# Kernel optimization log

Hardware: AMD Instinct MI355X
Metric: run time of the kernel (lower is better)

Reference implementation:

```python
import jax, jax.numpy as jnp
import numpy as np

WINDOW = 4
EPS = 1e-5


def setup_inputs() -> dict:
    key = jax.random.key(0)
    ks = jax.random.split(key, 12)
    B, T, D = 2, 4096, 1024
    H = D // 2
    s = 0.02
    return {
        "x": jax.random.normal(ks[0], (B, T, D), dtype=jnp.float32),
        # tension_net: Linear(2D -> D/2), SiLU, Linear(D/2 -> 1). Weights stored [in, out].
        "w1": jax.random.normal(ks[1], (2 * D, H), dtype=jnp.float32) * s,
        "b1": jnp.zeros((H,), dtype=jnp.float32),
        "w2": jax.random.normal(ks[2], (H, 1), dtype=jnp.float32) * s,
        "b2": jnp.zeros((1,), dtype=jnp.float32),
        # wv: Linear(D -> D)
        "wv_w": jax.random.normal(ks[3], (D, D), dtype=jnp.float32) * s,
        "wv_b": jnp.zeros((D,), dtype=jnp.float32),
        # merge: Linear(2D -> D)
        "merge_w": jax.random.normal(ks[4], (2 * D, D), dtype=jnp.float32) * s,
        "merge_b": jnp.zeros((D,), dtype=jnp.float32),
        # LayerNorm(D)
        "gamma": jnp.ones((D,), dtype=jnp.float32),
        "beta": jnp.zeros((D,), dtype=jnp.float32),
    }


def reference(x, w1, b1, w2, b2, wv_w, wv_b, merge_w, merge_b, gamma, beta):
    B, T, D = x.shape
    W = WINDOW
    # Causal sliding-window neighbor gather: nb[:, t, w] = x[:, t-w-1] if t-w-1 >= 0 else 0.
    idx = jnp.arange(T)[:, None] - jnp.arange(W)[None, :] - 1          # [T, W]
    valid = (idx >= 0)                                                  # [T, W]
    nb = jnp.take(x, jnp.clip(idx, 0, None), axis=1)                   # [B, T, W, D]
    nb = jnp.where(valid[None, :, :, None], nb, jnp.zeros((), x.dtype))
    # Pairwise tension gate: tiny MLP on [h_t, nb].
    h_t = jnp.broadcast_to(x[:, :, None, :], (B, T, W, D))
    pair = jnp.concatenate([h_t, nb], axis=-1)                          # [B, T, W, 2D]
    hid = jax.nn.silu(jnp.einsum('btwe,eh->btwh', pair, w1) + b1)       # [B, T, W, D/2]
    tau = jax.nn.sigmoid((jnp.einsum('btwh,ho->btwo', hid, w2) + b2)[..., 0])  # [B, T, W]
    # Value projection of neighbors (note: zero-padded neighbors still get wv bias, matching torch).
    v = jnp.einsum('btwd,de->btwe', nb, wv_w) + wv_b                    # [B, T, W, D]
    msg = jnp.einsum('btw,btwd->btd', tau, v)                           # [B, T, D]
    # Merge + LayerNorm.
    y = jnp.einsum('bte,ed->btd', jnp.concatenate([x, msg], axis=-1), merge_w) + merge_b
    mu = jnp.mean(y, axis=-1, keepdims=True)
    var = jnp.mean(jnp.square(y - mu), axis=-1, keepdims=True)
    y = (y - mu) * jax.lax.rsqrt(var + EPS) * gamma + beta
    return y
```

## Files before the change

kernel.cpp:

```cpp
#include <hip/hip_runtime.h>
#include <hip/hip_bf16.h>

#define TT 4096
#define TD 1024
#define TM 8192
#define CN 3072
#define EPS 1e-5f

typedef __bf16 bf16;
typedef __bf16 bf16x4 __attribute__((ext_vector_type(4)));
typedef __bf16 bf16x8 __attribute__((ext_vector_type(8)));
typedef float  f32x4  __attribute__((ext_vector_type(4)));

#define GLOBAL_AS __attribute__((address_space(1)))
#define LDS_AS    __attribute__((address_space(3)))

__global__ __launch_bounds__(256) void prep_kernel(const float* __restrict__ x,
                                                   const float* __restrict__ w1,
                                                   const float* __restrict__ wv_w,
                                                   const float* __restrict__ wv_b,
                                                   const float* __restrict__ merge_w,
                                                   bf16* __restrict__ Xbf,
                                                   bf16* __restrict__ BigBT,
                                                   bf16* __restrict__ Amb,
                                                   bf16* __restrict__ WvBf,
                                                   float* __restrict__ cvecP) {
    __shared__ float tile[32][33];
    int b = blockIdx.x;
    const int tid = threadIdx.x;

    if (b < 16) {
        const int j = (b & 3) * 256 + tid;
        const int e0 = (b >> 2) * 256;
        const float* col = merge_w + (size_t)(1024 + e0) * 1024 + j;
        float acc = 0.f;
#pragma unroll 32
        for (int e = 0; e < 256; ++e) acc += wv_b[e0 + e] * col[(size_t)e * 1024];
        cvecP[(b >> 2) * 1024 + j] = acc;
        return;
    }
    b -= 16;
    if (b < 8192) {
        int i = b * 256 + tid;
        float4 v = ((const float4*)x)[i];
        bf16x4 o; o[0] = (bf16)v.x; o[1] = (bf16)v.y; o[2] = (bf16)v.z; o[3] = (bf16)v.w;
        *(bf16x4*)(Xbf + (size_t)i * 4) = o;
        return;
    }
    b -= 8192;

    const float* src; bf16* dst; int srcN, tilesX, dstOff;
    if (b < 512)       {            src = w1;                        srcN = 512;  tilesX = 16; dst = BigBT; dstOff = 0;    }
    else if (b < 1024) { b -= 512;  src = w1 + (size_t)1024 * 512;   srcN = 512;  tilesX = 16; dst = BigBT; dstOff = 512;  }
    else if (b < 2048) { b -= 1024; src = merge_w;                   srcN = 1024; tilesX = 32; dst = BigBT; dstOff = 2048; }
    else if (b < 3072) { b -= 2048; src = merge_w + (size_t)1024 * 1024; srcN = 1024; tilesX = 32; dst = Amb; dstOff = 0; }
    else {
        b -= 3072;
        int i = b * 256 + tid;
        float4 v = ((const float4*)wv_w)[i];
        bf16x4 o; o[0] = (bf16)v.x; o[1] = (bf16)v.y; o[2] = (bf16)v.z; o[3] = (bf16)v.w;
        *(bf16x4*)(WvBf + (size_t)i * 4) = o;
        return;
    }
    int n0 = (b % tilesX) * 32, k0 = (b / tilesX) * 32;
    int tx = tid & 31, ty = tid >> 5;
#pragma unroll
    for (int r = 0; r < 32; r += 8)
        tile[ty + r][tx] = src[(size_t)(k0 + ty + r) * srcN + n0 + tx];
    __syncthreads();
#pragma unroll
    for (int r = 0; r < 32; r += 8)
        dst[(size_t)(dstOff + n0 + ty + r) * 1024 + k0 + tx] = (bf16)tile[tx][ty + r];
}

__global__ __launch_bounds__(256) void wprime_kernel(const bf16* __restrict__ Amb,
                                                     const bf16* __restrict__ WvBf,
                                                     bf16* __restrict__ Wout,
                                                     const float* __restrict__ cvecP,
                                                     float* __restrict__ cvec) {
    int b = blockIdx.x;
    if (b == 256) {
        int j = threadIdx.x * 4;
        float4 s0 = *(const float4*)(cvecP + j);
        float4 s1 = *(const float4*)(cvecP + 1024 + j);
        float4 s2 = *(const float4*)(cvecP + 2048 + j);
        float4 s3 = *(const float4*)(cvecP + 3072 + j);
        float4 o = {s0.x + s1.x + s2.x + s3.x, s0.y + s1.y + s2.y + s3.y,
                    s0.z + s1.z + s2.z + s3.z, s0.w + s1.w + s2.w + s3.w};
        *(float4*)(cvec + j) = o;
        return;
    }
    __shared__ bf16 As[64 * 64];
    __shared__ bf16 Bs[64 * 64];
    const int m0 = (b >> 4) * 64;
    const int n0 = (b & 15) * 64;
    const int tid = threadIdx.x;
    const int wave = tid >> 6, lane = tid & 63;
    const int wr = (wave >> 1) * 32, wc = (wave & 1) * 32;
    const int lrow = lane & 15, cbase = lane >> 4;
    const int sw = lrow & 7;

    f32x4 acc[2][2] = {};

    for (int k0 = 0; k0 < 1024; k0 += 64) {
        __syncthreads();
#pragma unroll
        for (int c = 0; c < 2; ++c) {
            int e = (c * 256 + tid) * 8;
            int row = e >> 6;
            int q = (e >> 3) & 7;
            int gcol = ((q ^ (row & 7)) << 3);
            const bf16* ga = Amb  + (size_t)(m0 + row) * 1024 + k0 + gcol;
            const bf16* gb = WvBf + (size_t)(n0 + row) * 1024 + k0 + gcol;
            __builtin_amdgcn_global_load_lds((const GLOBAL_AS void*)ga,
                                             (LDS_AS void*)(As + e), 16, 0, 0);
            __builtin_amdgcn_global_load_lds((const GLOBAL_AS void*)gb,
                                             (LDS_AS void*)(Bs + e), 16, 0, 0);
        }
        __syncthreads();

#pragma unroll
        for (int kk = 0; kk < 2; ++kk) {
            const int qo = ((cbase + kk * 4) ^ sw) << 3;
            bf16x8 af[2], bfr[2];
#pragma unroll
            for (int i = 0; i < 2; ++i) {
                af[i]  = *(const bf16x8*)(As + (wr + i * 16 + lrow) * 64 + qo);
                bfr[i] = *(const bf16x8*)(Bs + (wc + i * 16 + lrow) * 64 + qo);
            }
#pragma unroll
            for (int i = 0; i < 2; ++i)
#pragma unroll
                for (int j = 0; j < 2; ++j)
                    acc[i][j] = __builtin_amdgcn_mfma_f32_16x16x32_bf16(af[i], bfr[j], acc[i][j], 0, 0, 0);
        }
    }

    const int lr = (lane >> 4) * 4, lc = lane & 15;
#pragma unroll
    for (int i = 0; i < 2; ++i)
#pragma unroll
        for (int j = 0; j < 2; ++j)
#pragma unroll
            for (int r = 0; r < 4; ++r)
                Wout[(size_t)(m0 + wr + i * 16 + lr + r) * 1024 + (n0 + wc + j * 16 + lc)]
                    = (bf16)acc[i][j][r];
}

#define STAGE_A(T, kh) do {                                                       \
    bf16* base_ = SMEM + ((T) & 1) * 16384 + (kh) * 8192;                         \
    _Pragma("unroll")                                                             \
    for (int ld = 0; ld < 2; ++ld) {                                              \
        int e_ = (ld * 512 + tid) * 8;                                            \
        int row_ = e_ >> 5;                                                       \
        int q2_ = (e_ >> 3) & 3;                                                  \
        int gcol_ = ((q2_ ^ (row_ & 3)) << 3);                                    \
        const bf16* ga_ = A + (size_t)(m0 + row_) * K + (T) * 64 + (kh) * 32 + gcol_; \
        __builtin_amdgcn_global_load_lds((const GLOBAL_AS void*)ga_,              \
                                         (LDS_AS void*)(base_ + e_), 16, 0, 0);   \
    } } while (0)

#define STAGE_B(T) do {                                                           \
    bf16* base_ = SMEM + 32768 + ((T) & 1) * 12288;                               \
    _Pragma("unroll")                                                             \
    for (int ld = 0; ld < 3; ++ld) {                                              \
        int e_ = (ld * 512 + tid) * 8;                                            \
        int row_ = e_ >> 6;                                                       \
        int q_ = (e_ >> 3) & 7;                                                   \
        int gcol_ = ((q_ ^ (row_ & 7)) << 3);                                     \
        const bf16* gb_ = BT + (size_t)(n0 + row_) * K + (T) * 64 + gcol_;        \
        __builtin_amdgcn_global_load_lds((const GLOBAL_AS void*)gb_,              \
                                         (LDS_AS void*)(base_ + e_), 16, 0, 0);   \
    } } while (0)

#define NOSTAGE do {} while (0)
#define NOGATE  do {} while (0)
#define GATE2 do { asm volatile("s_waitcnt vmcnt(2)" ::: "memory");               \
                   __builtin_amdgcn_sched_barrier(0); } while (0)
#define GATE0 do { asm volatile("s_waitcnt vmcnt(0)" ::: "memory");               \
                   __builtin_amdgcn_sched_barrier(0); } while (0)

#define PHASE(tt, kk, ih, STAGE, GATE) do {                                       \
    bf16x8 af0 = *(const bf16x8*)(SMEM + (tt) * 16384 + (kk) * 8192 +             \
                                  (wm * 64 + (ih) * 32 + lrow) * 32 + aqo);       \
    bf16x8 af1 = *(const bf16x8*)(SMEM + (tt) * 16384 + (kk) * 8192 +             \
                                  (wm * 64 + (ih) * 32 + 16 + lrow) * 32 + aqo);  \
    if ((ih) == 0) {                                                              \
        _Pragma("unroll")                                                         \
        for (int j = 0; j < 6; ++j)                                               \
            bfr[j] = *(const bf16x8*)(SMEM + 32768 + (tt) * 12288 +               \
                                      (wn * 96 + j * 16 + lrow) * 64 +            \
                                      (((cbase + (kk) * 4) ^ sw) << 3));          \
    }                                                                             \
    STAGE;                                                                        \
    __builtin_amdgcn_s_barrier();                                                 \
    __builtin_amdgcn_sched_barrier(0);                                            \
    __builtin_amdgcn_s_setprio(1);                                                \
    _Pragma("unroll")                                                             \
    for (int j = 0; j < 6; ++j) {                                                 \
        acc[(ih) * 2][j]     = __builtin_amdgcn_mfma_f32_16x16x32_bf16(           \
                                   af0, bfr[j], acc[(ih) * 2][j], 0, 0, 0);       \
        acc[(ih) * 2 + 1][j] = __builtin_amdgcn_mfma_f32_16x16x32_bf16(           \
                                   af1, bfr[j], acc[(ih) * 2 + 1][j], 0, 0, 0);   \
    }                                                                             \
    __builtin_amdgcn_s_setprio(0);                                                \
    GATE;                                                                         \
    __builtin_amdgcn_s_barrier();                                                 \
    __builtin_amdgcn_sched_barrier(0);                                            \
} while (0)

__global__ __launch_bounds__(512, 2) void gemm_big(const bf16* __restrict__ A,
                                                   const bf16* __restrict__ BT,
                                                   bf16* __restrict__ C) {
    __shared__ __align__(16) bf16 SMEM[57344];
    const int NB = 3072, K = 1024;

    int L = blockIdx.y * 16 + blockIdx.x;
    int tile = (L & 7) * 64 + (L >> 3);
    const int m0 = (tile >> 4) * 256;
    const int n0 = (tile & 15) * 192;
    const int tid = threadIdx.x;
    const int wave = tid >> 6, lane = tid & 63;
    const int wm = wave >> 1;
    const int wn = wave & 1;
    const int lrow = lane & 15, cbase = lane >> 4;
    const int sw = lrow & 7;
    const int aqo = ((cbase ^ (lrow & 3)) << 3);

    f32x4 acc[4][6] = {};
    bf16x8 bfr[6];

    STAGE_A(0, 0);
    STAGE_A(0, 1);
    STAGE_B(0);
    STAGE_A(1, 0);
    asm volatile("s_waitcnt vmcnt(2)" ::: "memory");
    __builtin_amdgcn_sched_barrier(0);
    __builtin_amdgcn_s_barrier();
    __builtin_amdgcn_sched_barrier(0);

    for (int i = 0; i < 7; ++i) {
        const int t1 = 2 * i + 1, t2 = 2 * i + 2, t3 = 2 * i + 3;
        PHASE(0, 0, 0, STAGE_A(t1, 1), NOGATE);
        PHASE(0, 0, 1, STAGE_B(t1),    NOGATE);
        PHASE(0, 1, 0, STAGE_A(t2, 0), NOGATE);
        PHASE(0, 1, 1, NOSTAGE,        GATE2);
        PHASE(1, 0, 0, STAGE_A(t2, 1), NOGATE);
        PHASE(1, 0, 1, STAGE_B(t2),    NOGATE);
        PHASE(1, 1, 0, STAGE_A(t3, 0), NOGATE);
        PHASE(1, 1, 1, NOSTAGE,        GATE2);
    }
    PHASE(0, 0, 0, STAGE_A(15, 1), NOGATE);
    PHASE(0, 0, 1, STAGE_B(15),    NOGATE);
    PHASE(0, 1, 0, NOSTAGE,        NOGATE);
    PHASE(0, 1, 1, NOSTAGE,        GATE0);
    PHASE(1, 0, 0, NOSTAGE,        NOGATE);
    PHASE(1, 0, 1, NOSTAGE,        NOGATE);
    PHASE(1, 1, 0, NOSTAGE,        NOGATE);
    PHASE(1, 1, 1, NOSTAGE,        NOGATE);

    __syncthreads();
    bf16* ep = SMEM + wave * 6656;
    const int lr = (lane >> 4) * 4, lc = lane & 15;
#pragma unroll
    for (int i = 0; i < 4; ++i)
#pragma unroll
        for (int j = 0; j < 6; ++j)
#pragma unroll
            for (int r = 0; r < 4; ++r)
                ep[(i * 16 + lr + r) * 104 + (j * 16 + lc)] = (bf16)acc[i][j][r];
    __syncthreads();

    bf16* Cw = C + (size_t)(m0 + wm * 64) * NB + n0 + wn * 96;
#pragma unroll
    for (int p = 0; p < 8; ++p) {
        int R = p * 8 + (lane >> 3);
        int Ccol = (lane & 7) * 8;
        bf16x8 v = *(const bf16x8*)(ep + R * 104 + Ccol);
        *(bf16x8*)(Cw + (size_t)R * NB + Ccol) = v;
    }
#pragma unroll
    for (int p = 0; p < 4; ++p) {
        int R = p * 16 + (lane >> 2);
        int Ccol = 64 + (lane & 3) * 8;
        bf16x8 v = *(const bf16x8*)(ep + R * 104 + Ccol);
        *(bf16x8*)(Cw + (size_t)R * NB + Ccol) = v;
    }
}

__global__ __launch_bounds__(256) void final_kernel(const bf16* __restrict__ C,
                                                    const float* __restrict__ b1,
                                                    const float* __restrict__ b2,
                                                    const float* __restrict__ w2,
                                                    const float* __restrict__ cvec,
                                                    const float* __restrict__ merge_b,
                                                    const float* __restrict__ gamma,
                                                    const float* __restrict__ beta,
                                                    float* __restrict__ out) {
    const int wave = threadIdx.x >> 6, lane = threadIdx.x & 63;
    const int row = blockIdx.x * 4 + wave;
    const int t = row & (TT - 1);
    const bf16* Crow = C + (size_t)row * CN;

    const int h0 = lane * 8;
    bf16x8 u8 = *(const bf16x8*)(Crow + h0);
    float4 b1a = *(const float4*)(b1 + h0), b1b = *(const float4*)(b1 + h0 + 4);
    float4 w2a = *(const float4*)(w2 + h0), w2b = *(const float4*)(w2 + h0 + 4);
    float u[8] = {(float)u8[0] + b1a.x, (float)u8[1] + b1a.y,
                  (float)u8[2] + b1a.z, (float)u8[3] + b1a.w,
                  (float)u8[4] + b1b.x, (float)u8[5] + b1b.y,
                  (float)u8[6] + b1b.z, (float)u8[7] + b1b.w};
    const float w2v[8] = {w2a.x, w2a.y, w2a.z, w2a.w, w2b.x, w2b.y, w2b.z, w2b.w};

    float partial[4];
#pragma unroll
    for (int w = 0; w < 4; ++w) {
        float p = 0.f;
        if (t >= w + 1) {
            bf16x8 v8 = *(const bf16x8*)(C + (size_t)(row - w - 1) * CN + 512 + h0);
#pragma unroll
            for (int k = 0; k < 8; ++k) {
                float z = u[k] + (float)v8[k];
                p += (z / (1.f + __expf(-z))) * w2v[k];
            }
        } else {
#pragma unroll
            for (int k = 0; k < 8; ++k) {
                float z = u[k];
                p += (z / (1.f + __expf(-z))) * w2v[k];
            }
        }
        partial[w] = p;
    }
#pragma unroll
    for (int w = 0; w < 4; ++w)
#pragma unroll
        for (int off = 1; off < 64; off <<= 1)
            partial[w] += __shfl_xor(partial[w], off, 64);

    const float bias2 = b2[0];
    float taus[4];
#pragma unroll
    for (int w = 0; w < 4; ++w)
        taus[w] = 1.f / (1.f + __expf(-(partial[w] + bias2)));
    const float tsum = taus[0] + taus[1] + taus[2] + taus[3];

    const int d0 = lane * 16;
    bf16x8 y1a = *(const bf16x8*)(Crow + 2048 + d0);
    bf16x8 y1b = *(const bf16x8*)(Crow + 2048 + d0 + 8);
    float v[16];
#pragma unroll
    for (int k = 0; k < 8; ++k) { v[k] = (float)y1a[k]; v[8 + k] = (float)y1b[k]; }
#pragma unroll
    for (int q = 0; q < 4; ++q) {
        float4 cv = *(const float4*)(cvec + d0 + q * 4);
        float4 mb = *(const float4*)(merge_b + d0 + q * 4);
        v[q*4+0] += tsum * cv.x + mb.x; v[q*4+1] += tsum * cv.y + mb.y;
        v[q*4+2] += tsum * cv.z + mb.z; v[q*4+3] += tsum * cv.w + mb.w;
    }
#pragma unroll
    for (int w = 0; w < 4; ++w) {
        if (t >= w + 1) {
            const bf16* Pn = C + (size_t)(row - w - 1) * CN + 1024 + d0;
            bf16x8 pa = *(const bf16x8*)Pn;
            bf16x8 pb = *(const bf16x8*)(Pn + 8);
#pragma unroll
            for (int k = 0; k < 8; ++k) {
                v[k] += taus[w] * (float)pa[k];
                v[8 + k] += taus[w] * (float)pb[k];
            }
        }
    }

    float s = 0.f, ss = 0.f;
#pragma unroll
    for (int k = 0; k < 16; ++k) { s += v[k]; ss += v[k] * v[k]; }
#pragma unroll
    for (int off = 1; off < 64; off <<= 1) {
        s  += __shfl_xor(s, off, 64);
        ss += __shfl_xor(ss, off, 64);
    }
    const float mu = s * (1.f / TD);
    const float var = ss * (1.f / TD) - mu * mu;
    const float r = rsqrtf(var + EPS);

#pragma unroll
    for (int q = 0; q < 4; ++q) {
        float4 g  = *(const float4*)(gamma + d0 + q * 4);
        float4 bt = *(const float4*)(beta + d0 + q * 4);
        float4 o;
        o.x = (v[q*4+0] - mu) * r * g.x + bt.x;
        o.y = (v[q*4+1] - mu) * r * g.y + bt.y;
        o.z = (v[q*4+2] - mu) * r * g.z + bt.z;
        o.w = (v[q*4+3] - mu) * r * g.w + bt.w;
        *(float4*)(out + (size_t)row * TD + d0 + q * 4) = o;
    }
}

extern "C" void kernel_launch(void* const* d_in, const int* in_sizes, int n_in,
                              void* d_out, int out_size, void* d_ws, size_t ws_size,
                              hipStream_t stream) {
    const float* x       = (const float*)d_in[0];
    const float* w1      = (const float*)d_in[1];
    const float* b1      = (const float*)d_in[2];
    const float* w2      = (const float*)d_in[3];
    const float* b2      = (const float*)d_in[4];
    const float* wv_w    = (const float*)d_in[5];
    const float* wv_b    = (const float*)d_in[6];
    const float* merge_w = (const float*)d_in[7];
    const float* merge_b = (const float*)d_in[8];
    const float* gamma   = (const float*)d_in[9];
    const float* beta    = (const float*)d_in[10];
    float* out = (float*)d_out;

    char* ws = (char*)d_ws;
    bf16*  Xbf   = (bf16*)ws;  ws += (size_t)TM * 1024 * 2;
    bf16*  BigBT = (bf16*)ws;  ws += (size_t)CN * 1024 * 2;
    bf16*  Amb   = (bf16*)ws;  ws += (size_t)1024 * 1024 * 2;
    bf16*  WvBf  = (bf16*)ws;  ws += (size_t)1024 * 1024 * 2;
    float* cvecP = (float*)ws; ws += (size_t)4 * 1024 * 4;
    float* cvec  = (float*)ws; ws += (size_t)1024 * 4;
    bf16*  Cbuf  = (bf16*)ws;

    prep_kernel<<<12304, 256, 0, stream>>>(x, w1, wv_w, wv_b, merge_w,
                                           Xbf, BigBT, Amb, WvBf, cvecP);

    wprime_kernel<<<257, 256, 0, stream>>>(Amb, WvBf, BigBT + (size_t)1024 * 1024,
                                           cvecP, cvec);

    gemm_big<<<dim3(16, 32), 512, 0, stream>>>(Xbf, BigBT, Cbuf);

    final_kernel<<<TM / 4, 256, 0, stream>>>(Cbuf, b1, b2, w2, cvec, merge_b,
                                             gamma, beta, out);
}
```

Baseline: 202.7 us.

## Enlarge big GEMM tile to 256x384 with full-K-tile double buffering

```diff
diff --git a/kernel.cpp b/kernel.cpp
--- a/kernel.cpp
+++ b/kernel.cpp
@@ -147,61 +147,53 @@
                     = (bf16)acc[i][j][r];
 }
 
-#define STAGE_A(T, kh) do {                                                       \
-    bf16* base_ = SMEM + ((T) & 1) * 16384 + (kh) * 8192;                         \
+#define MFMA16(a, b, c) __builtin_amdgcn_mfma_f32_16x16x32_bf16((a), (b), (c), 0, 0, 0)
+
+#define STAGE_A(BUF, T) do {                                                      \
     _Pragma("unroll")                                                             \
-    for (int ld = 0; ld < 2; ++ld) {                                              \
-        int e_ = (ld * 512 + tid) * 8;                                            \
-        int row_ = e_ >> 5;                                                       \
-        int q2_ = (e_ >> 3) & 3;                                                  \
-        int gcol_ = ((q2_ ^ (row_ & 3)) << 3);                                    \
-        const bf16* ga_ = A + (size_t)(m0 + row_) * K + (T) * 64 + (kh) * 32 + gcol_; \
+    for (int ld_ = 0; ld_ < 4; ++ld_) {                                           \
+        const bf16* ga_ = aBase + (size_t)(ld_ * 64) * 1024 + (T) * 64;           \
         __builtin_amdgcn_global_load_lds((const GLOBAL_AS void*)ga_,              \
-                                         (LDS_AS void*)(base_ + e_), 16, 0, 0);   \
+            (LDS_AS void*)(SMEM + (BUF) * 40960 + ld_ * 4096 + tid * 8), 16, 0, 0); \
     } } while (0)
 
-#define STAGE_B(T) do {                                                           \
-    bf16* base_ = SMEM + 32768 + ((T) & 1) * 12288;                               \
+#define STAGE_B(BUF, T, L0, L1) do {                                              \
     _Pragma("unroll")                                                             \
-    for (int ld = 0; ld < 3; ++ld) {                                              \
-        int e_ = (ld * 512 + tid) * 8;                                            \
-        int row_ = e_ >> 6;                                                       \
-        int q_ = (e_ >> 3) & 7;                                                   \
-        int gcol_ = ((q_ ^ (row_ & 7)) << 3);                                     \
-        const bf16* gb_ = BT + (size_t)(n0 + row_) * K + (T) * 64 + gcol_;        \
+    for (int ld_ = (L0); ld_ < (L1); ++ld_) {                                     \
+        const bf16* gb_ = bBase + (size_t)(ld_ * 64) * 1024 + (T) * 64;           \
         __builtin_amdgcn_global_load_lds((const GLOBAL_AS void*)gb_,              \
-                                         (LDS_AS void*)(base_ + e_), 16, 0, 0);   \
+            (LDS_AS void*)(SMEM + (BUF) * 40960 + 16384 + ld_ * 4096 + tid * 8), 16, 0, 0); \
     } } while (0)
+
+#define AF(BUF, I, KK) (*(const bf16x8*)(SMEM + (BUF) * 40960 +                   \
+    (wm * 128 + (I) * 16 + lrow) * 64 + (((cbase + (KK) * 4) ^ sw) << 3)))
+#define BF(BUF, J, KK) (*(const bf16x8*)(SMEM + (BUF) * 40960 + 16384 +           \
+    (wn * 96 + (J) * 16 + lrow) * 64 + (((cbase + (KK) * 4) ^ sw) << 3)))
 
 #define NOSTAGE do {} while (0)
 #define NOGATE  do {} while (0)
-#define GATE2 do { asm volatile("s_waitcnt vmcnt(2)" ::: "memory");               \
-                   __builtin_amdgcn_sched_barrier(0); } while (0)
 #define GATE0 do { asm volatile("s_waitcnt vmcnt(0)" ::: "memory");               \
                    __builtin_amdgcn_sched_barrier(0); } while (0)
 
-#define PHASE(tt, kk, ih, STAGE, GATE) do {                                       \
-    bf16x8 af0 = *(const bf16x8*)(SMEM + (tt) * 16384 + (kk) * 8192 +             \
-                                  (wm * 64 + (ih) * 32 + lrow) * 32 + aqo);       \
-    bf16x8 af1 = *(const bf16x8*)(SMEM + (tt) * 16384 + (kk) * 8192 +             \
-                                  (wm * 64 + (ih) * 32 + 16 + lrow) * 32 + aqo);  \
-    if ((ih) == 0) {                                                              \
+#define PH(BUF, KK, H, RDB, STAGE, GATE) do {                                     \
+    if (RDB) {                                                                    \
         _Pragma("unroll")                                                         \
-        for (int j = 0; j < 6; ++j)                                               \
-            bfr[j] = *(const bf16x8*)(SMEM + 32768 + (tt) * 12288 +               \
-                                      (wn * 96 + j * 16 + lrow) * 64 +            \
-                                      (((cbase + (kk) * 4) ^ sw) << 3));          \
+        for (int j = 0; j < 6; ++j) bfr[j] = BF(BUF, j, KK);                      \
     }                                                                             \
+    bf16x8 a0_ = AF(BUF, (H) * 4 + 0, KK);                                        \
+    bf16x8 a1_ = AF(BUF, (H) * 4 + 1, KK);                                        \
+    bf16x8 a2_ = AF(BUF, (H) * 4 + 2, KK);                                        \
+    bf16x8 a3_ = AF(BUF, (H) * 4 + 3, KK);                                        \
     STAGE;                                                                        \
     __builtin_amdgcn_s_barrier();                                                 \
     __builtin_amdgcn_sched_barrier(0);                                            \
     __builtin_amdgcn_s_setprio(1);                                                \
     _Pragma("unroll")                                                             \
     for (int j = 0; j < 6; ++j) {                                                 \
-        acc[(ih) * 2][j]     = __builtin_amdgcn_mfma_f32_16x16x32_bf16(           \
-                                   af0, bfr[j], acc[(ih) * 2][j], 0, 0, 0);       \
-        acc[(ih) * 2 + 1][j] = __builtin_amdgcn_mfma_f32_16x16x32_bf16(           \
-                                   af1, bfr[j], acc[(ih) * 2 + 1][j], 0, 0, 0);   \
+        acc[(H) * 4 + 0][j] = MFMA16(a0_, bfr[j], acc[(H) * 4 + 0][j]);           \
+        acc[(H) * 4 + 1][j] = MFMA16(a1_, bfr[j], acc[(H) * 4 + 1][j]);           \
+        acc[(H) * 4 + 2][j] = MFMA16(a2_, bfr[j], acc[(H) * 4 + 2][j]);           \
+        acc[(H) * 4 + 3][j] = MFMA16(a3_, bfr[j], acc[(H) * 4 + 3][j]);           \
     }                                                                             \
     __builtin_amdgcn_s_setprio(0);                                                \
     GATE;                                                                         \
@@ -209,82 +201,81 @@
     __builtin_amdgcn_sched_barrier(0);                                            \
 } while (0)
 
+#define TILE(BUF, S0, S1, S2, G3)                                                 \
+    PH(BUF, 0, 0, 1, S0, NOGATE);                                                 \
+    PH(BUF, 0, 1, 0, S1, NOGATE);                                                 \
+    PH(BUF, 1, 0, 1, S2, NOGATE);                                                 \
+    PH(BUF, 1, 1, 0, NOSTAGE, G3);
+
 __global__ __launch_bounds__(512, 2) void gemm_big(const bf16* __restrict__ A,
                                                    const bf16* __restrict__ BT,
                                                    bf16* __restrict__ C) {
-    __shared__ __align__(16) bf16 SMEM[57344];
+    __shared__ __align__(16) bf16 SMEM[81920];
     const int NB = 3072, K = 1024;
 
-    int L = blockIdx.y * 16 + blockIdx.x;
-    int tile = (L & 7) * 64 + (L >> 3);
-    const int m0 = (tile >> 4) * 256;
-    const int n0 = (tile & 15) * 192;
+    const int L = blockIdx.x;
+    const int m0 = (L >> 3) * 256;
+    const int n0 = (L & 7) * 384;
     const int tid = threadIdx.x;
     const int wave = tid >> 6, lane = tid & 63;
-    const int wm = wave >> 1;
-    const int wn = wave & 1;
+    const int wm = wave >> 2;
+    const int wn = wave & 3;
     const int lrow = lane & 15, cbase = lane >> 4;
     const int sw = lrow & 7;
-    const int aqo = ((cbase ^ (lrow & 3)) << 3);
-
-    f32x4 acc[4][6] = {};
+
+    const int r0 = tid >> 3;
+    const int c0 = ((tid & 7) ^ ((tid >> 3) & 7)) << 3;
+    const bf16* aBase = A  + (size_t)(m0 + r0) * K + c0;
+    const bf16* bBase = BT + (size_t)(n0 + r0) * K + c0;
+
+    f32x4 acc[8][6] = {};
     bf16x8 bfr[6];
 
     STAGE_A(0, 0);
-    STAGE_A(0, 1);
-    STAGE_B(0);
-    STAGE_A(1, 0);
-    asm volatile("s_waitcnt vmcnt(2)" ::: "memory");
+    STAGE_B(0, 0, 0, 6);
+    asm volatile("s_waitcnt vmcnt(0)" ::: "memory");
     __builtin_amdgcn_sched_barrier(0);
     __builtin_amdgcn_s_barrier();
     __builtin_amdgcn_sched_barrier(0);
 
     for (int i = 0; i < 7; ++i) {
-        const int t1 = 2 * i + 1, t2 = 2 * i + 2, t3 = 2 * i + 3;
-        PHASE(0, 0, 0, STAGE_A(t1, 1), NOGATE);
-        PHASE(0, 0, 1, STAGE_B(t1),    NOGATE);
-        PHASE(0, 1, 0, STAGE_A(t2, 0), NOGATE);
-        PHASE(0, 1, 1, NOSTAGE,        GATE2);
-        PHASE(1, 0, 0, STAGE_A(t2, 1), NOGATE);
-        PHASE(1, 0, 1, STAGE_B(t2),    NOGATE);
-        PHASE(1, 1, 0, STAGE_A(t3, 0), NOGATE);
-        PHASE(1, 1, 1, NOSTAGE,        GATE2);
-    }
-    PHASE(0, 0, 0, STAGE_A(15, 1), NOGATE);
-    PHASE(0, 0, 1, STAGE_B(15),    NOGATE);
-    PHASE(0, 1, 0, NOSTAGE,        NOGATE);
-    PHASE(0, 1, 1, NOSTAGE,        GATE0);
-    PHASE(1, 0, 0, NOSTAGE,        NOGATE);
-    PHASE(1, 0, 1, NOSTAGE,        NOGATE);
-    PHASE(1, 1, 0, NOSTAGE,        NOGATE);
-    PHASE(1, 1, 1, NOSTAGE,        NOGATE);
+        const int t1 = 2 * i + 1, t2 = 2 * i + 2;
+        TILE(0, STAGE_A(1, t1), STAGE_B(1, t1, 0, 3), STAGE_B(1, t1, 3, 6), GATE0);
+        TILE(1, STAGE_A(0, t2), STAGE_B(0, t2, 0, 3), STAGE_B(0, t2, 3, 6), GATE0);
+    }
+    TILE(0, STAGE_A(1, 15), STAGE_B(1, 15, 0, 3), STAGE_B(1, 15, 3, 6), GATE0);
+    TILE(1, NOSTAGE, NOSTAGE, NOSTAGE, NOGATE);
 
     __syncthreads();
     bf16* ep = SMEM + wave * 6656;
     const int lr = (lane >> 4) * 4, lc = lane & 15;
 #pragma unroll
-    for (int i = 0; i < 4; ++i)
-#pragma unroll
-        for (int j = 0; j < 6; ++j)
-#pragma unroll
-            for (int r = 0; r < 4; ++r)
-                ep[(i * 16 + lr + r) * 104 + (j * 16 + lc)] = (bf16)acc[i][j][r];
-    __syncthreads();
-
-    bf16* Cw = C + (size_t)(m0 + wm * 64) * NB + n0 + wn * 96;
-#pragma unroll
-    for (int p = 0; p < 8; ++p) {
-        int R = p * 8 + (lane >> 3);
-        int Ccol = (lane & 7) * 8;
-        bf16x8 v = *(const bf16x8*)(ep + R * 104 + Ccol);
-        *(bf16x8*)(Cw + (size_t)R * NB + Ccol) = v;
-    }
-#pragma unroll
-    for (int p = 0; p < 4; ++p) {
-        int R = p * 16 + (lane >> 2);
-        int Ccol = 64 + (lane & 3) * 8;
-        bf16x8 v = *(const bf16x8*)(ep + R * 104 + Ccol);
-        *(bf16x8*)(Cw + (size_t)R * NB + Ccol) = v;
+    for (int h = 0; h < 2; ++h) {
+#pragma unroll
+        for (int ii = 0; ii < 4; ++ii)
+#pragma unroll
+            for (int j = 0; j < 6; ++j)
+#pragma unroll
+                for (int r = 0; r < 4; ++r)
+                    ep[(ii * 16 + lr + r) * 104 + (j * 16 + lc)]
+                        = (bf16)acc[h * 4 + ii][j][r];
+        __syncthreads();
+        bf16* Cw = C + (size_t)(m0 + wm * 128 + h * 64) * NB + n0 + wn * 96;
+#pragma unroll
+        for (int p = 0; p < 8; ++p) {
+            int R = p * 8 + (lane >> 3);
+            int Ccol = (lane & 7) * 8;
+            bf16x8 v = *(const bf16x8*)(ep + R * 104 + Ccol);
+            *(bf16x8*)(Cw + (size_t)R * NB + Ccol) = v;
+        }
+#pragma unroll
+        for (int p = 0; p < 4; ++p) {
+            int R = p * 16 + (lane >> 2);
+            int Ccol = 64 + (lane & 3) * 8;
+            bf16x8 v = *(const bf16x8*)(ep + R * 104 + Ccol);
+            *(bf16x8*)(Cw + (size_t)R * NB + Ccol) = v;
+        }
+        __syncthreads();
     }
 }
 
@@ -428,7 +419,7 @@
     wprime_kernel<<<257, 256, 0, stream>>>(Amb, WvBf, BigBT + (size_t)1024 * 1024,
                                            cvecP, cvec);
 
-    gemm_big<<<dim3(16, 32), 512, 0, stream>>>(Xbf, BigBT, Cbuf);
+    gemm_big<<<256, 512, 0, stream>>>(Xbf, BigBT, Cbuf);
 
     final_kernel<<<TM / 4, 256, 0, stream>>>(Cbuf, b1, b2, w2, cvec, merge_b,
                                              gamma, beta, out);
```

Result: slower. 207.7 us (+2.5%).
